# Optimization experiments

Measured on AMD Instinct MI355X. Metric: run time of the kernel, lower is better.

Reference implementation:

```python
import jax, jax.numpy as jnp
import numpy as np

N_HEAD = 16

def _phi(x):
    # silu(x) + 1 feature map
    return jax.nn.silu(x) + 1.0

def setup_inputs() -> dict:
    key = jax.random.key(0)
    ks = jax.random.split(key, 8)
    B, T, D = 8, 4096, 1024
    s = 0.02
    return {
        "x":  jax.random.normal(ks[0], (B, T, D), jnp.float32),
        "Wq": jax.random.normal(ks[1], (D, D), jnp.float32) * s,
        "bq": jax.random.normal(ks[2], (D,), jnp.float32) * s,
        "Wk": jax.random.normal(ks[3], (D, D), jnp.float32) * s,
        "Wv": jax.random.normal(ks[4], (D, D), jnp.float32) * s,
        "bv": jax.random.normal(ks[5], (D,), jnp.float32) * s,
        "Wo": jax.random.normal(ks[6], (D, D), jnp.float32) * s,
        "bo": jax.random.normal(ks[7], (D,), jnp.float32) * s,
    }

def reference(x, Wq, bq, Wk, Wv, bv, Wo, bo):
    B, T, D = x.shape
    H = N_HEAD
    Dh = D // H
    scale = Dh ** (-0.25)
    # projections (torch F.linear: x @ W.T + b); key has no bias
    q = x @ Wq.T + bq
    k = x @ Wk.T
    v = x @ Wv.T + bv
    # [B, T, H, Dh] -> [B, H, T, Dh]
    q = q.reshape(B, T, H, Dh).transpose(0, 2, 1, 3) * scale
    k = k.reshape(B, T, H, Dh).transpose(0, 2, 1, 3) * scale
    v = v.reshape(B, T, H, Dh).transpose(0, 2, 1, 3)
    phi_q = _phi(q)
    phi_k = _phi(k)
    # kv: [B, H, Dh, Dh] = sum_t phi_k[t]^T v[t]
    kv = jnp.einsum('bhtd,bhte->bhde', phi_k, v)
    out = jnp.einsum('bhtd,bhde->bhte', phi_q, kv)  # [B, H, T, Dh]
    wv = out.transpose(0, 2, 1, 3).reshape(B, T, D)
    return wv @ Wo.T + bo
```

## Files before the change

### kernel.cpp

```cpp
#include <hip/hip_runtime.h>
#include <math.h>

typedef short bf16x8 __attribute__((ext_vector_type(8)));
typedef float f32x4  __attribute__((ext_vector_type(4)));

__device__ __forceinline__ float phi_act(float t) {
    return t / (1.0f + __expf(-t)) + 1.0f;
}

__device__ __forceinline__ unsigned short f2bf(float f) {
    union { float f; unsigned int u; } un; un.f = f;
    unsigned int r = un.u + 0x7fffu + ((un.u >> 16) & 1u);
    return (unsigned short)(r >> 16);
}

__device__ __forceinline__ void gload_lds16(const void* g, void* l) {
    __builtin_amdgcn_global_load_lds(
        (const __attribute__((address_space(1))) void*)g,
        (__attribute__((address_space(3))) void*)l, 16, 0, 0);
}


__device__ __forceinline__ void stage_half(const unsigned short* __restrict__ g,
                                           unsigned short* l, int tid) {
    const int wb = tid & ~63;
    #pragma unroll
    for (int u = 0; u < 2; u++) {
        const int p  = (u * 512 + tid) * 16;
        const int qq = p ^ (((p >> 7) & 7) << 4);
        gload_lds16((const char*)g + (size_t)(qq >> 7) * 2048 + (qq & 127),
                    (char*)l + (size_t)(u * 512 + wb) * 16);
    }
}

#define LOAD_AF(buf, ah) do {                                                   \
    const char* _s = (const char*)&As[buf][ah][0];                              \
    _Pragma("unroll")                                                           \
    for (int _mi = 0; _mi < 4; _mi++) {                                         \
        const int _row = qm * 64 + _mi * 16 + ml;                               \
        const int _sw = (_row & 7) << 4;                                        \
        _Pragma("unroll")                                                       \
        for (int _ks = 0; _ks < 2; _ks++)                                       \
            af[_mi][_ks] = *(const bf16x8*)(_s +                                \
                (((_row * 128) + _ks * 64 + kq * 16) ^ _sw));                   \
    }                                                                           \
} while (0)

#define LOAD_BF(buf, bh) do {                                                   \
    const char* _s = (const char*)&Bs[buf][bh][0];                              \
    _Pragma("unroll")                                                           \
    for (int _nj = 0; _nj < 2; _nj++) {                                         \
        const int _col = qn * 32 + _nj * 16 + ml;                               \
        const int _sw = (_col & 7) << 4;                                        \
        _Pragma("unroll")                                                       \
        for (int _ks = 0; _ks < 2; _ks++)                                       \
            bf[_nj][_ks] = *(const bf16x8*)(_s +                                \
                (((_col * 128) + _ks * 64 + kq * 16) ^ _sw));                   \
    }                                                                           \
} while (0)

#define MFMA_Q(Q) do {                                                          \
    __builtin_amdgcn_s_setprio(1);                                              \
    _Pragma("unroll")                                                           \
    for (int _mi = 0; _mi < 4; _mi++)                                           \
        _Pragma("unroll")                                                       \
        for (int _nj = 0; _nj < 2; _nj++)                                       \
            _Pragma("unroll")                                                   \
            for (int _ks = 0; _ks < 2; _ks++)                                   \
                acc[Q][_mi][_nj] = __builtin_amdgcn_mfma_f32_16x16x32_bf16(     \
                    af[_mi][_ks], bf[_nj][_ks], acc[Q][_mi][_nj], 0, 0, 0);     \
    __builtin_amdgcn_s_setprio(0);                                              \
} while (0)

template<int KIND>
__device__ __forceinline__ void gemm256_body(
    const unsigned short* __restrict__ A, const unsigned short* __restrict__ W,
    const float* __restrict__ bq, const float* __restrict__ bv,
    unsigned short* __restrict__ oq, unsigned short* __restrict__ okk,
    unsigned short* __restrict__ ov, float* __restrict__ outF,
    const float* __restrict__ bo, float scale, int NBN)
{
    __shared__ __align__(128) unsigned short As[2][2][128 * 64];
    __shared__ __align__(128) unsigned short Bs[2][2][128 * 64];

    const int tid  = threadIdx.x;
    const int lane = tid & 63;
    const int w    = tid >> 6;
    const int qm   = w >> 2;
    const int qn   = w & 3;
    const int ml   = lane & 15;
    const int kq   = lane >> 4;

    const int nwg  = (int)gridDim.x;
    const int bid  = (int)blockIdx.x;
    const int sbid = (bid & 7) * (nwg >> 3) + (bid >> 3);
    const int bn   = sbid % NBN;
    const int bm   = sbid / NBN;

    const unsigned short* Ab = A + (size_t)bm * 256 * 1024;
    const unsigned short* Bb = W + (size_t)bn * 256 * 1024;

    f32x4 acc[4][4][2];
    f32x4 zero4 = {0.f, 0.f, 0.f, 0.f};
    #pragma unroll
    for (int q = 0; q < 4; q++)
        #pragma unroll
        for (int mi = 0; mi < 4; mi++)
            #pragma unroll
            for (int nj = 0; nj < 2; nj++) acc[q][mi][nj] = zero4;

    bf16x8 af[4][2], bf[2][2];

    stage_half(Ab,                   &As[0][0][0], tid);
    stage_half(Ab + 128 * 1024,      &As[0][1][0], tid);
    stage_half(Bb,                   &Bs[0][0][0], tid);
    stage_half(Bb + 128 * 1024,      &Bs[0][1][0], tid);
    stage_half(Ab + 64,              &As[1][0][0], tid);

    for (int t = 0; t < 16; ++t) {
        const int buf = t & 1;
        if (t == 15) { asm volatile("s_waitcnt vmcnt(0)" ::: "memory"); }
        else         { asm volatile("s_waitcnt vmcnt(2)" ::: "memory"); }
        __builtin_amdgcn_s_barrier();
        asm volatile("" ::: "memory");

        if (t + 1 < 16) {
            stage_half(Ab + 128 * 1024 + (t + 1) * 64, &As[buf ^ 1][1][0], tid);
            stage_half(Bb + (t + 1) * 64,              &Bs[buf ^ 1][0][0], tid);
            stage_half(Bb + 128 * 1024 + (t + 1) * 64, &Bs[buf ^ 1][1][0], tid);
        }

        LOAD_AF(buf, 0);
        LOAD_BF(buf, 0);
        MFMA_Q(0);
        LOAD_BF(buf, 1);
        MFMA_Q(1);

        asm volatile("s_waitcnt lgkmcnt(0)" ::: "memory");
        __builtin_amdgcn_s_barrier();
        asm volatile("" ::: "memory");

        if (t + 2 < 16) stage_half(Ab + (t + 2) * 64, &As[buf][0][0], tid);

        LOAD_AF(buf, 1);
        LOAD_BF(buf, 1);
        MFMA_Q(2);
        LOAD_BF(buf, 0);
        MFMA_Q(3);

        asm volatile("s_waitcnt lgkmcnt(0)" ::: "memory");
    }

    const int rq = lane >> 4, cl = lane & 15;
    #pragma unroll
    for (int q = 0; q < 4; q++) {
        const int qr = (q >> 1) * 128;
        const int qc = ((q == 1) || (q == 2)) ? 128 : 0;
        #pragma unroll
        for (int nj = 0; nj < 2; nj++) {
            const int colg = bn * 256 + qc + qn * 32 + nj * 16 + cl;
            if constexpr (KIND == 0) {
                const int z    = colg >> 10;
                const int lcol = colg & 1023;
                const float bias = (z == 0) ? bq[lcol] : ((z == 2) ? bv[lcol] : 0.f);
                unsigned short* dst = (z == 0) ? oq : ((z == 1) ? okk : ov);
                #pragma unroll
                for (int mi = 0; mi < 4; mi++) {
                    const int row0 = bm * 256 + qr + qm * 64 + mi * 16 + rq * 4;
                    #pragma unroll
                    for (int r = 0; r < 4; r++) {
                        float vv = acc[q][mi][nj][r] + bias;
                        if (z < 2) vv = phi_act(vv * scale);
                        dst[(size_t)(row0 + r) * 1024 + lcol] = f2bf(vv);
                    }
                }
            } else {
                const float bias = bo[colg];
                #pragma unroll
                for (int mi = 0; mi < 4; mi++) {
                    const int row0 = bm * 256 + qr + qm * 64 + mi * 16 + rq * 4;
                    #pragma unroll
                    for (int r = 0; r < 4; r++)
                        outF[(size_t)(row0 + r) * 1024 + colg] = acc[q][mi][nj][r] + bias;
                }
            }
        }
    }
}

__global__ __launch_bounds__(512, 2) void qkv_gemm256(
    const unsigned short* __restrict__ xb,
    const unsigned short* __restrict__ wcat,
    const float* __restrict__ bq, const float* __restrict__ bv,
    unsigned short* __restrict__ phiq, unsigned short* __restrict__ phik,
    unsigned short* __restrict__ vb, float scale)
{
    gemm256_body<0>(xb, wcat, bq, bv, phiq, phik, vb, nullptr, nullptr, scale, 12);
}

__global__ __launch_bounds__(512, 2) void out_gemm256(
    const unsigned short* __restrict__ A, const unsigned short* __restrict__ W,
    const float* __restrict__ bo, float* __restrict__ out)
{
    gemm256_body<1>(A, W, nullptr, nullptr, nullptr, nullptr, nullptr, out, bo, 1.0f, 4);
}

__global__ __launch_bounds__(256) void cast_all(
    const float* __restrict__ x,  unsigned short* __restrict__ xb,
    const float* __restrict__ w0, unsigned short* __restrict__ w0b,
    const float* __restrict__ w1, unsigned short* __restrict__ w1b,
    const float* __restrict__ w2, unsigned short* __restrict__ w2b,
    const float* __restrict__ w3, unsigned short* __restrict__ w3b,
    size_t nx, size_t nw)
{
    size_t i = ((size_t)blockIdx.x * 256 + threadIdx.x) * 4;
    const float* s; unsigned short* d; size_t off;
    if (i < nx)               { s = x;  d = xb;  off = i; }
    else if (i < nx + nw)     { s = w0; d = w0b; off = i - nx; }
    else if (i < nx + 2 * nw) { s = w1; d = w1b; off = i - nx - nw; }
    else if (i < nx + 3 * nw) { s = w2; d = w2b; off = i - nx - 2 * nw; }
    else                      { s = w3; d = w3b; off = i - nx - 3 * nw; }
    float4 v = *(const float4*)(s + off);
    ushort4 o;
    o.x = f2bf(v.x); o.y = f2bf(v.y); o.z = f2bf(v.z); o.w = f2bf(v.w);
    *(ushort4*)(d + off) = o;
}

__global__ __launch_bounds__(256) void kv_part(
    const unsigned short* __restrict__ phiK, const unsigned short* __restrict__ V,
    float* __restrict__ partial, int Ttot, int D)
{
    const int tc = blockIdx.x, bh = blockIdx.y;
    const int b = bh >> 4, h = bh & 15;
    const int tbase = tc * 512;

    __shared__ unsigned short pkT[64][72];
    __shared__ unsigned short vvT[64][72];

    const int tid  = threadIdx.x;
    const int lane = tid & 63;
    const int w    = tid >> 6;
    const int dq = w >> 1, eq = w & 1;
    const int kq = lane >> 4, ml = lane & 15;

    f32x4 zero4 = {0.f, 0.f, 0.f, 0.f};
    f32x4 acc[2][2];
    acc[0][0] = zero4; acc[0][1] = zero4; acc[1][0] = zero4; acc[1][1] = zero4;

    const size_t base = (size_t)b * Ttot * D + h * 64;

    for (int c8 = 0; c8 < 8; c8++) {
        const int t0 = tbase + c8 * 64;
        __syncthreads();
        #pragma unroll
        for (int u = 0; u < 2; u++) {
            const int f = tid * 2 + u;
            const int trow = f >> 3;
            const int d8 = (f & 7) * 8;
            const size_t g = base + (size_t)(t0 + trow) * D + d8;
            uint4 kk = *(const uint4*)(phiK + g);
            uint4 vv = *(const uint4*)(V + g);
            pkT[d8 + 0][trow] = (unsigned short)(kk.x & 0xffff);
            pkT[d8 + 1][trow] = (unsigned short)(kk.x >> 16);
            pkT[d8 + 2][trow] = (unsigned short)(kk.y & 0xffff);
            pkT[d8 + 3][trow] = (unsigned short)(kk.y >> 16);
            pkT[d8 + 4][trow] = (unsigned short)(kk.z & 0xffff);
            pkT[d8 + 5][trow] = (unsigned short)(kk.z >> 16);
            pkT[d8 + 6][trow] = (unsigned short)(kk.w & 0xffff);
            pkT[d8 + 7][trow] = (unsigned short)(kk.w >> 16);
            vvT[d8 + 0][trow] = (unsigned short)(vv.x & 0xffff);
            vvT[d8 + 1][trow] = (unsigned short)(vv.x >> 16);
            vvT[d8 + 2][trow] = (unsigned short)(vv.y & 0xffff);
            vvT[d8 + 3][trow] = (unsigned short)(vv.y >> 16);
            vvT[d8 + 4][trow] = (unsigned short)(vv.z & 0xffff);
            vvT[d8 + 5][trow] = (unsigned short)(vv.z >> 16);
            vvT[d8 + 6][trow] = (unsigned short)(vv.w & 0xffff);
            vvT[d8 + 7][trow] = (unsigned short)(vv.w >> 16);
        }
        __syncthreads();

        #pragma unroll
        for (int ks = 0; ks < 2; ks++) {
            bf16x8 af[2], bfv[2];
            #pragma unroll
            for (int ai = 0; ai < 2; ai++)
                af[ai] = *(const bf16x8*)&pkT[dq * 32 + ai * 16 + ml][ks * 32 + kq * 8];
            #pragma unroll
            for (int bi = 0; bi < 2; bi++)
                bfv[bi] = *(const bf16x8*)&vvT[eq * 32 + bi * 16 + ml][ks * 32 + kq * 8];
            #pragma unroll
            for (int ai = 0; ai < 2; ai++)
                #pragma unroll
                for (int bi = 0; bi < 2; bi++)
                    acc[ai][bi] = __builtin_amdgcn_mfma_f32_16x16x32_bf16(
                        af[ai], bfv[bi], acc[ai][bi], 0, 0, 0);
        }
    }

    float* outp = partial + ((size_t)bh * 8 + tc) * 4096;
    const int rq = lane >> 4, cl = lane & 15;
    #pragma unroll
    for (int ai = 0; ai < 2; ai++)
        #pragma unroll
        for (int bi = 0; bi < 2; bi++) {
            const int e = eq * 32 + bi * 16 + cl;
            #pragma unroll
            for (int r = 0; r < 4; r++) {
                const int d = dq * 32 + ai * 16 + rq * 4 + r;
                outp[d * 64 + e] = acc[ai][bi][r];
            }
        }
}

__global__ __launch_bounds__(256) void kv_reduce(
    const float* __restrict__ partial, unsigned short* __restrict__ kvT)
{
    const int bh = blockIdx.x;
    const int tid = threadIdx.x;
    __shared__ float s[64][65];
    float a[16];
    #pragma unroll
    for (int c = 0; c < 16; c++) a[c] = 0.f;
    #pragma unroll
    for (int p = 0; p < 8; p++) {
        const float* src = partial + ((size_t)bh * 8 + p) * 4096;
        #pragma unroll
        for (int c = 0; c < 16; c++) a[c] += src[c * 256 + tid];
    }
    #pragma unroll
    for (int c = 0; c < 16; c++) {
        const int idx = c * 256 + tid;
        s[idx >> 6][idx & 63] = a[c];
    }
    __syncthreads();
    unsigned short* outp = kvT + (size_t)bh * 4096;
    #pragma unroll
    for (int c = 0; c < 16; c++) {
        const int j = c * 256 + tid;
        outp[j] = f2bf(s[j & 63][j >> 6]);
    }
}

__global__ __launch_bounds__(256) void av_mfma(
    const unsigned short* __restrict__ phiQ, const unsigned short* __restrict__ kvT,
    unsigned short* __restrict__ Oattn, int Ttot, int D)
{
    const int bh = blockIdx.y;
    const int b = bh >> 4, h = bh & 15;
    const int t0 = blockIdx.x * 256;

    __shared__ unsigned short Aq[256 * 64];
    __shared__ unsigned short Kv[64][72];

    const int tid  = threadIdx.x;
    const int lane = tid & 63;
    const int w    = tid >> 6;
    const int kq = lane >> 4, ml = lane & 15;

    {
        const int e = tid >> 2;
        const int c16 = (tid & 3) * 16;
        const unsigned short* src = kvT + (size_t)bh * 4096 + e * 64 + c16;
        *(uint4*)&Kv[e][c16]     = *(const uint4*)(src);
        *(uint4*)&Kv[e][c16 + 8] = *(const uint4*)(src + 8);
    }
    {
        const int lr = lane >> 3;
        const int d8 = (lane & 7) * 8;
        #pragma unroll
        for (int r = 0; r < 8; r++) {
            const int chunk = r * 4 + w;
            const int row = chunk * 8 + lr;
            gload_lds16(phiQ + ((size_t)(b * Ttot + t0 + row)) * D + h * 64 + d8,
                        &Aq[chunk * 512]);
        }
    }
    __syncthreads();

    f32x4 zero4 = {0.f, 0.f, 0.f, 0.f};
    f32x4 acc[4][4];
    #pragma unroll
    for (int i = 0; i < 4; i++)
        #pragma unroll
        for (int j = 0; j < 4; j++) acc[i][j] = zero4;

    #pragma unroll
    for (int ks = 0; ks < 2; ks++) {
        bf16x8 af[4], bfv[4];
        #pragma unroll
        for (int mi = 0; mi < 4; mi++)
            af[mi] = *(const bf16x8*)&Aq[(w * 64 + mi * 16 + ml) * 64 + ks * 32 + kq * 8];
        #pragma unroll
        for (int nj = 0; nj < 4; nj++)
            bfv[nj] = *(const bf16x8*)&Kv[nj * 16 + ml][ks * 32 + kq * 8];
        #pragma unroll
        for (int mi = 0; mi < 4; mi++)
            #pragma unroll
            for (int nj = 0; nj < 4; nj++)
                acc[mi][nj] = __builtin_amdgcn_mfma_f32_16x16x32_bf16(
                    af[mi], bfv[nj], acc[mi][nj], 0, 0, 0);
    }

    const int rq = lane >> 4, cl = lane & 15;
    #pragma unroll
    for (int mi = 0; mi < 4; mi++) {
        #pragma unroll
        for (int r = 0; r < 4; r++) {
            const int t = t0 + w * 64 + mi * 16 + rq * 4 + r;
            unsigned short* dst = Oattn + (size_t)(b * Ttot + t) * D + h * 64;
            #pragma unroll
            for (int nj = 0; nj < 4; nj++)
                dst[nj * 16 + cl] = f2bf(acc[mi][nj][r]);
        }
    }
}

extern "C" void kernel_launch(void* const* d_in, const int* in_sizes, int n_in,
                              void* d_out, int out_size, void* d_ws, size_t ws_size,
                              hipStream_t stream) {
    const float* x  = (const float*)d_in[0];
    const float* Wq = (const float*)d_in[1];
    const float* bq = (const float*)d_in[2];
    const float* Wk = (const float*)d_in[3];
    const float* Wv = (const float*)d_in[4];
    const float* bv = (const float*)d_in[5];
    const float* Wo = (const float*)d_in[6];
    const float* bo = (const float*)d_in[7];
    float* out = (float*)d_out;

    const int B = 8, T = 4096, D = 1024;
    const int M = B * T;
    const float scale = 0.35355339059327379f;
    const size_t MD = (size_t)M * D;
    const size_t WN = (size_t)D * D;

    unsigned short* xb    = (unsigned short*)d_ws;
    unsigned short* wqb   = xb + MD;
    unsigned short* wkb   = wqb + WN;
    unsigned short* wvb   = wkb + WN;
    unsigned short* wob   = wvb + WN;
    unsigned short* phiq  = wob + WN;
    unsigned short* phik  = phiq + MD;
    unsigned short* vb    = phik + MD;
    unsigned short* oat   = vb + MD;
    float*          part  = (float*)(oat + MD);
    unsigned short* kvT   = (unsigned short*)(part + (size_t)1024 * 4096);
    (void)ws_size; (void)in_sizes; (void)n_in; (void)out_size;

    dim3 blk(256);

    {
        size_t total4 = (MD + 4 * WN) / 4;
        cast_all<<<dim3((unsigned)(total4 / 256)), blk, 0, stream>>>(
            x, xb, Wq, wqb, Wk, wkb, Wv, wvb, Wo, wob, MD, WN);
    }

    qkv_gemm256<<<dim3(1536), dim3(512), 0, stream>>>(
        xb, wqb, bq, bv, phiq, phik, vb, scale);

    kv_part<<<dim3(8, 128), blk, 0, stream>>>(phik, vb, part, T, D);
    kv_reduce<<<dim3(128), blk, 0, stream>>>(part, kvT);

    av_mfma<<<dim3(T / 256, 128), blk, 0, stream>>>(phiq, kvT, oat, T, D);

    out_gemm256<<<dim3(512), dim3(512), 0, stream>>>(oat, wob, bo, out);
}
```

Baseline: 668.7 us.

## Restructure GEMM main loop into three-phase staged prefetch with B fragments kept in registers

The bf16 GEMM main loop now issues global-to-LDS prefetches for the next K tile in three phases, each followed by its own vmcnt wait and barrier, instead of one bulk issue per iteration plus a separate refill of the other A half. Both B-fragment halves are held in separate register sets (bf0, bf1), so each is read from LDS once per K step rather than twice. Per-thread global offsets are now computed once, outside the loop. The goal is fewer redundant LDS reads and finer overlap of global loads with MFMA work, at the cost of more vector registers and one extra barrier per iteration.

```diff
diff --git a/kernel.cpp b/kernel.cpp
--- a/kernel.cpp
+++ b/kernel.cpp
@@ -21,16 +21,10 @@
 }
 
 
-__device__ __forceinline__ void stage_half(const unsigned short* __restrict__ g,
-                                           unsigned short* l, int tid) {
-    const int wb = tid & ~63;
-    #pragma unroll
-    for (int u = 0; u < 2; u++) {
-        const int p  = (u * 512 + tid) * 16;
-        const int qq = p ^ (((p >> 7) & 7) << 4);
-        gload_lds16((const char*)g + (size_t)(qq >> 7) * 2048 + (qq & 127),
-                    (char*)l + (size_t)(u * 512 + wb) * 16);
-    }
+__device__ __forceinline__ void stage2(const char* g, int voff0, int voff1,
+                                       char* l, int wb16) {
+    gload_lds16(g + voff0, l + wb16);
+    gload_lds16(g + voff1, l + 8192 + wb16);
 }
 
 #define LOAD_AF(buf, ah) do {                                                   \
@@ -46,7 +40,7 @@
     }                                                                           \
 } while (0)
 
-#define LOAD_BF(buf, bh) do {                                                   \
+#define LOAD_BF_TO(dst, buf, bh) do {                                           \
     const char* _s = (const char*)&Bs[buf][bh][0];                              \
     _Pragma("unroll")                                                           \
     for (int _nj = 0; _nj < 2; _nj++) {                                         \
@@ -54,12 +48,12 @@
         const int _sw = (_col & 7) << 4;                                        \
         _Pragma("unroll")                                                       \
         for (int _ks = 0; _ks < 2; _ks++)                                       \
-            bf[_nj][_ks] = *(const bf16x8*)(_s +                                \
+            dst[_nj][_ks] = *(const bf16x8*)(_s +                               \
                 (((_col * 128) + _ks * 64 + kq * 16) ^ _sw));                   \
     }                                                                           \
 } while (0)
 
-#define MFMA_Q(Q) do {                                                          \
+#define MFMA_Q(Q, B) do {                                                       \
     __builtin_amdgcn_s_setprio(1);                                              \
     _Pragma("unroll")                                                           \
     for (int _mi = 0; _mi < 4; _mi++)                                           \
@@ -68,7 +62,7 @@
             _Pragma("unroll")                                                   \
             for (int _ks = 0; _ks < 2; _ks++)                                   \
                 acc[Q][_mi][_nj] = __builtin_amdgcn_mfma_f32_16x16x32_bf16(     \
-                    af[_mi][_ks], bf[_nj][_ks], acc[Q][_mi][_nj], 0, 0, 0);     \
+                    af[_mi][_ks], B[_nj][_ks], acc[Q][_mi][_nj], 0, 0, 0);      \
     __builtin_amdgcn_s_setprio(0);                                              \
 } while (0)
 
@@ -97,8 +91,17 @@
     const int bn   = sbid % NBN;
     const int bm   = sbid / NBN;
 
-    const unsigned short* Ab = A + (size_t)bm * 256 * 1024;
-    const unsigned short* Bb = W + (size_t)bn * 256 * 1024;
+    const char* pA = (const char*)(A + (size_t)bm * 256 * 1024);
+    const char* pB = (const char*)(W + (size_t)bn * 256 * 1024);
+
+    int voff[2];
+    #pragma unroll
+    for (int u = 0; u < 2; u++) {
+        const int p  = (u * 512 + tid) * 16;
+        const int qq = p ^ (((p >> 7) & 7) << 4);
+        voff[u] = (qq >> 7) * 2048 + (qq & 127);
+    }
+    const int wb16 = (tid & ~63) * 16;
 
     f32x4 acc[4][4][2];
     f32x4 zero4 = {0.f, 0.f, 0.f, 0.f};
@@ -109,46 +112,52 @@
             #pragma unroll
             for (int nj = 0; nj < 2; nj++) acc[q][mi][nj] = zero4;
 
-    bf16x8 af[4][2], bf[2][2];
-
-    stage_half(Ab,                   &As[0][0][0], tid);
-    stage_half(Ab + 128 * 1024,      &As[0][1][0], tid);
-    stage_half(Bb,                   &Bs[0][0][0], tid);
-    stage_half(Bb + 128 * 1024,      &Bs[0][1][0], tid);
-    stage_half(Ab + 64,              &As[1][0][0], tid);
+    bf16x8 af[4][2], bf0[2][2], bf1[2][2];
+
+    stage2(pA,              voff[0], voff[1], (char*)&As[0][0][0], wb16);
+    stage2(pB,              voff[0], voff[1], (char*)&Bs[0][0][0], wb16);
+    stage2(pB + 256 * 1024, voff[0], voff[1], (char*)&Bs[0][1][0], wb16);
+    stage2(pA + 256 * 1024, voff[0], voff[1], (char*)&As[0][1][0], wb16);
 
     for (int t = 0; t < 16; ++t) {
         const int buf = t & 1;
-        if (t == 15) { asm volatile("s_waitcnt vmcnt(0)" ::: "memory"); }
-        else         { asm volatile("s_waitcnt vmcnt(2)" ::: "memory"); }
+        const char* A0n = pA + (size_t)(t + 1) * 128;
+        const char* A1n = A0n + 256 * 1024;
+        const char* B0n = pB + (size_t)(t + 1) * 128;
+        const char* B1n = B0n + 256 * 1024;
+        const bool st = (t + 1 < 16);
+
+        asm volatile("s_waitcnt vmcnt(4)" ::: "memory");
         __builtin_amdgcn_s_barrier();
         asm volatile("" ::: "memory");
-
-        if (t + 1 < 16) {
-            stage_half(Ab + 128 * 1024 + (t + 1) * 64, &As[buf ^ 1][1][0], tid);
-            stage_half(Bb + (t + 1) * 64,              &Bs[buf ^ 1][0][0], tid);
-            stage_half(Bb + 128 * 1024 + (t + 1) * 64, &Bs[buf ^ 1][1][0], tid);
-        }
-
         LOAD_AF(buf, 0);
-        LOAD_BF(buf, 0);
-        MFMA_Q(0);
-        LOAD_BF(buf, 1);
-        MFMA_Q(1);
-
+        LOAD_BF_TO(bf0, buf, 0);
+        if (st) {
+            stage2(A0n, voff[0], voff[1], (char*)&As[buf ^ 1][0][0], wb16);
+            stage2(B0n, voff[0], voff[1], (char*)&Bs[buf ^ 1][0][0], wb16);
+        }
         asm volatile("s_waitcnt lgkmcnt(0)" ::: "memory");
+        MFMA_Q(0, bf0);
+
+        if (st) { asm volatile("s_waitcnt vmcnt(6)" ::: "memory"); }
+        else    { asm volatile("s_waitcnt vmcnt(2)" ::: "memory"); }
         __builtin_amdgcn_s_barrier();
         asm volatile("" ::: "memory");
-
-        if (t + 2 < 16) stage_half(Ab + (t + 2) * 64, &As[buf][0][0], tid);
-
+        LOAD_BF_TO(bf1, buf, 1);
+        if (st) stage2(B1n, voff[0], voff[1], (char*)&Bs[buf ^ 1][1][0], wb16);
+        asm volatile("s_waitcnt lgkmcnt(0)" ::: "memory");
+        MFMA_Q(1, bf1);
+
+        if (st) { asm volatile("s_waitcnt vmcnt(6)" ::: "memory"); }
+        else    { asm volatile("s_waitcnt vmcnt(0)" ::: "memory"); }
+        __builtin_amdgcn_s_barrier();
+        asm volatile("" ::: "memory");
         LOAD_AF(buf, 1);
-        LOAD_BF(buf, 1);
-        MFMA_Q(2);
-        LOAD_BF(buf, 0);
-        MFMA_Q(3);
-
+        if (st) stage2(A1n, voff[0], voff[1], (char*)&As[buf ^ 1][1][0], wb16);
         asm volatile("s_waitcnt lgkmcnt(0)" ::: "memory");
+        MFMA_Q(2, bf1);
+
+        MFMA_Q(3, bf0);
     }
 
     const int rq = lane >> 4, cl = lane & 15;
```

Measured after the change: 608.9 us. 8.9% less time.
